# Kernel tuning notes

Hardware: AMD Instinct MI355X
Metric: run time of the kernel (lower is better)

The kernel has to match this reference:

```python
import jax, jax.numpy as jnp
import numpy as np

FEATURE_DIM = 256
TEMP = 0.1
BASE_TEMP = 0.07
MAX_SAMPLES = 1024
SIM_THR = 0.7


def setup_inputs() -> dict:
    key = jax.random.key(0)
    ks = jax.random.split(key, 8)
    B, C, H, W = 4, FEATURE_DIM, 160, 160
    s = 1.0 / np.sqrt(C)
    return {
        'feats': jax.random.normal(ks[0], (B, C, H, W), jnp.float32),
        'labels': jax.random.randint(ks[1], (B, H, W), 0, 2).astype(jnp.int64),
        'superpixel_indice': jax.random.randint(ks[2], (B, H, W), 0, 200).astype(jnp.int64),
        'w1': jax.random.normal(ks[3], (C, C), jnp.float32) * s,
        'b1': jnp.zeros((C,), jnp.float32),
        'w2': jax.random.normal(ks[4], (C, C), jnp.float32) * s,
        'b2': jnp.zeros((C,), jnp.float32),
        'wa1': jax.random.normal(ks[5], (64, C), jnp.float32) * s,
        'ba1': jnp.zeros((64,), jnp.float32),
        'wa2': jax.random.normal(ks[6], (1, 64), jnp.float32) * (1.0 / 8.0),
        'ba2': jnp.zeros((1,), jnp.float32),
    }


def _per_sample(f, w, lab, sp):
    # f: (N, C) normalized proj feats, w: (N,) pixel weights, lab/sp: (N,) int
    valid = lab == 1
    # deterministic sample: stable-sort valid pixels to the front, take MAX_SAMPLES
    order = jnp.argsort(jnp.where(valid, 0, 1).astype(jnp.int32))
    idx = order[:MAX_SAMPLES]
    sel = valid[idx]                       # (S,) real-sample mask (pads if <S valid)
    tf = f[idx]                            # (S, C)
    tw = w[idx]                            # (S,)
    ts = sp[idx]                           # (S,)
    sim = tf @ tf.T                        # (S, S)
    S = MAX_SAMPLES
    eye = jnp.eye(S, dtype=bool)
    pos = (ts[:, None] == ts[None, :]) & (sim > SIM_THR)
    pos = pos & sel[:, None] & sel[None, :] & ~eye
    exp_sim = jnp.exp(sim / TEMP) * sel[None, :].astype(sim.dtype)
    denom = exp_sim.sum(axis=1)            # (S,)
    log_prob = sim / TEMP - jnp.log(jnp.where(denom > 0, denom, 1.0))[:, None]
    pw = tw[:, None] * tw[None, :]
    pwm = jnp.where(pos, pw, 0.0)
    psum = pwm.sum()
    loss = -(TEMP / BASE_TEMP) * (pwm * jnp.where(pos, log_prob, 0.0)).sum() / jnp.where(psum > 0, psum, 1.0)
    has = psum > 0
    return jnp.where(has, loss, 0.0), has


def reference(feats, labels, superpixel_indice, w1, b1, w2, b2, wa1, ba1, wa2, ba2):
    B, C, H, W = feats.shape
    x = jnp.transpose(feats, (0, 2, 3, 1)).reshape(B, H * W, C)  # (B, N, C)
    proj = jax.nn.relu(x @ w1.T + b1) @ w2.T + b2                # 1x1 convs == per-pixel matmul
    attn = jax.nn.sigmoid(jax.nn.relu(x @ wa1.T + ba1) @ wa2.T + ba2)[..., 0]  # (B, N)
    nrm = jnp.linalg.norm(proj, axis=-1, keepdims=True)
    fn = proj / jnp.maximum(nrm, 1e-12)
    lab = labels.reshape(B, -1)
    sp = superpixel_indice.reshape(B, -1)
    losses, flags = jax.vmap(_per_sample)(fn, attn, lab, sp)
    n = flags.sum().astype(jnp.float32)
    return jnp.where(n > 0, losses.sum() / jnp.maximum(n, 1.0), 0.0)
```

## Files before the change

kernel.cpp:

```cpp
#include <hip/hip_runtime.h>
#include <hip/hip_bf16.h>
#include <math.h>

#define NPIX   25600
#define CDIM   256
#define SSEL   1024
#define BATCH  4
#define NCHUNK 25
#define INV_T  10.0f
#define RATIO  1.4285714285714286f
#define THR    0.7f

typedef __attribute__((ext_vector_type(8))) short bf16x8;
typedef __attribute__((ext_vector_type(4))) float f32x4;
typedef unsigned short u16;

__device__ __forceinline__ u16 to_bf16(float v) {
  __hip_bfloat16 h = __float2bfloat16(v);
  return *reinterpret_cast<u16*>(&h);
}

__global__ __launch_bounds__(256) void pack_weights(
    const float* __restrict__ w1, const float* __restrict__ w2,
    const float* __restrict__ wa1, const int* __restrict__ labels,
    u16* __restrict__ w1b, u16* __restrict__ w2b, u16* __restrict__ wab,
    float* __restrict__ denom, float* __restrict__ Prow, float* __restrict__ Ssum,
    int* __restrict__ counts) {
  int t = threadIdx.x;
  int e = blockIdx.x * 256 + t;
  if (e < 65536) {
    w1b[e] = to_bf16(w1[e]);
    w2b[e] = to_bf16(w2[e]);
  }
  if (e < 16384) wab[e] = to_bf16(wa1[e]);
  if (e < BATCH * SSEL) { denom[e] = 0.f; Prow[e] = 0.f; }
  if (e < BATCH) Ssum[e] = 0.f;

  if (blockIdx.x < BATCH * NCHUNK) {
    int b = blockIdx.x / NCHUNK, ch = blockIdx.x % NCHUNK;
    const int* lab = labels + b * NPIX + ch * 1024;
    int local = 0;
#pragma unroll
    for (int qq = 0; qq < 4; ++qq) local += (lab[qq * 256 + t] == 1);
    for (int off = 32; off > 0; off >>= 1) local += __shfl_xor(local, off, 64);
    __shared__ int ws[4];
    if ((t & 63) == 0) ws[t >> 6] = local;
    __syncthreads();
    if (t == 0) counts[blockIdx.x] = ws[0] + ws[1] + ws[2] + ws[3];
  }
}

__global__ __launch_bounds__(1024) void select_scatter(
    const int* __restrict__ labels, const int* __restrict__ sp,
    const int* __restrict__ counts,
    int* __restrict__ idx, int* __restrict__ selv, int* __restrict__ tsp) {
  int b = blockIdx.x / NCHUNK, ch = blockIdx.x % NCHUNK;
  int t = threadIdx.x;
  __shared__ int cs[NCHUNK];
  __shared__ int wave_tot[16];
  if (t < NCHUNK) cs[t] = counts[b * NCHUNK + t];
  __syncthreads();
  int Vtot = 0, vbase = 0;
#pragma unroll
  for (int c = 0; c < NCHUNK; ++c) {
    int v = cs[c];
    Vtot += v;
    if (c < ch) vbase += v;
  }
  int ibase = ch * 1024 - vbase;

  int i = ch * 1024 + t;
  int isv = (labels[b * NPIX + i] == 1) ? 1 : 0;
  int lane = t & 63, wid = t >> 6;
  unsigned long long mv = __ballot(isv);
  int pv = __popcll(mv & ((1ull << lane) - 1ull));
  if (lane == 0) wave_tot[wid] = __popcll(mv);
  __syncthreads();
  for (int w = 0; w < wid; ++w) pv += wave_tot[w];
  int gslot = isv ? (vbase + pv) : (Vtot + ibase + (t - pv));
  if (gslot < SSEL) {
    idx [b * SSEL + gslot] = i;
    selv[b * SSEL + gslot] = isv;
    tsp [b * SSEL + gslot] = sp[b * NPIX + i];
  }
}

__global__ __launch_bounds__(256) void gather_cast(
    const float* __restrict__ feats, const int* __restrict__ idx,
    u16* __restrict__ xh) {
  int r0 = blockIdx.x * 16;
  int b  = r0 >> 10;
  int t  = threadIdx.x;
  __shared__ int ridx[16];
  if (t < 16) ridx[t] = idx[r0 + t];
  __syncthreads();
  const float* fb = feats + ((long)b * CDIM + t) * NPIX;
#pragma unroll 4
  for (int r = 0; r < 16; ++r) {
    xh[(long)(r0 + r) * CDIM + t] = to_bf16(fb[ridx[r]]);
  }
}

__global__ __launch_bounds__(256) void gemm1_kernel(
    const u16* __restrict__ xh, const u16* __restrict__ w1b,
    const u16* __restrict__ wab,
    const float* __restrict__ b1, const float* __restrict__ ba1,
    const float* __restrict__ wa2, const float* __restrict__ ba2,
    u16* __restrict__ hh, float* __restrict__ tw) {
  int n  = blockIdx.x;
  int i0 = blockIdx.y * 64;
  int t = threadIdx.x;
  int lane = t & 63, w = t >> 6, m = lane & 15, q = lane >> 4;
  bool attn = (n == 4);
  const u16* bsrc = attn ? wab : (w1b + n * 64 * 256);

  __shared__ __align__(16) u16 Ah[64 * 72];
  __shared__ __align__(16) u16 Bh[64 * 72];

  f32x4 acc[4];
#pragma unroll
  for (int nt = 0; nt < 4; ++nt) acc[nt] = {0.f, 0.f, 0.f, 0.f};

  for (int kk = 0; kk < 4; ++kk) {
    __syncthreads();
#pragma unroll
    for (int p = 0; p < 2; ++p) {
      int e = p * 256 + t;
      int row = e >> 3, kg = e & 7;
      int lo = row * 72 + kg * 8;
      *(uint4*)&Ah[lo] = *(const uint4*)&xh[(i0 + row) * 256 + kk * 64 + kg * 8];
      *(uint4*)&Bh[lo] = *(const uint4*)&bsrc[row * 256 + kk * 64 + kg * 8];
    }
    __syncthreads();
#pragma unroll
    for (int ks = 0; ks < 2; ++ks) {
      int koff = ks * 32 + q * 8;
      bf16x8 ah = *(const bf16x8*)&Ah[(w * 16 + m) * 72 + koff];
#pragma unroll
      for (int nt = 0; nt < 4; ++nt) {
        bf16x8 bh = *(const bf16x8*)&Bh[(nt * 16 + m) * 72 + koff];
        acc[nt] = __builtin_amdgcn_mfma_f32_16x16x32_bf16(ah, bh, acc[nt], 0, 0, 0);
      }
    }
  }

  if (!attn) {
#pragma unroll
    for (int nt = 0; nt < 4; ++nt) {
      int col = n * 64 + nt * 16 + m;
      float bb = b1[col];
#pragma unroll
      for (int reg = 0; reg < 4; ++reg) {
        int row = i0 + w * 16 + q * 4 + reg;
        hh[row * 256 + col] = to_bf16(fmaxf(acc[nt][reg] + bb, 0.f));
      }
    }
  } else {
    float part[4] = {0.f, 0.f, 0.f, 0.f};
#pragma unroll
    for (int nt = 0; nt < 4; ++nt) {
      int ca = nt * 16 + m;
      float bb = ba1[ca], wv = wa2[ca];
#pragma unroll
      for (int reg = 0; reg < 4; ++reg)
        part[reg] += fmaxf(acc[nt][reg] + bb, 0.f) * wv;
    }
    for (int off = 8; off > 0; off >>= 1) {
#pragma unroll
      for (int reg = 0; reg < 4; ++reg)
        part[reg] += __shfl_xor(part[reg], off, 64);
    }
    if (m == 0) {
      float bb2 = ba2[0];
#pragma unroll
      for (int reg = 0; reg < 4; ++reg) {
        int row = i0 + w * 16 + q * 4 + reg;
        tw[row] = 1.f / (1.f + expf(-(part[reg] + bb2)));
      }
    }
  }
}

__global__ __launch_bounds__(256) void gemm2norm_kernel(
    const u16* __restrict__ hh, const u16* __restrict__ w2b,
    const float* __restrict__ b2, u16* __restrict__ fnb) {
  int i0 = blockIdx.x * 64;
  int t = threadIdx.x;
  int lane = t & 63, w = t >> 6, m = lane & 15, q = lane >> 4;

  __shared__ __align__(16) u16 Bs[64 * 264];

  bf16x8 af[8];
#pragma unroll
  for (int ks = 0; ks < 8; ++ks)
    af[ks] = *(const bf16x8*)&hh[(i0 + w * 16 + m) * 256 + ks * 32 + q * 8];

  f32x4 acc[4][4];
#pragma unroll
  for (int n = 0; n < 4; ++n)
#pragma unroll
    for (int nt = 0; nt < 4; ++nt) acc[n][nt] = {0.f, 0.f, 0.f, 0.f};

  for (int n = 0; n < 4; ++n) {
    __syncthreads();
#pragma unroll
    for (int i = 0; i < 8; ++i) {
      int e = i * 256 + t;
      int row = e >> 5, kg = e & 31;
      *(uint4*)&Bs[row * 264 + kg * 8] = *(const uint4*)&w2b[(n * 64 + row) * 256 + kg * 8];
    }
    __syncthreads();
#pragma unroll
    for (int ks = 0; ks < 8; ++ks) {
      int koff = ks * 32 + q * 8;
#pragma unroll
      for (int nt = 0; nt < 4; ++nt) {
        bf16x8 bh = *(const bf16x8*)&Bs[(nt * 16 + m) * 264 + koff];
        acc[n][nt] = __builtin_amdgcn_mfma_f32_16x16x32_bf16(af[ks], bh, acc[n][nt], 0, 0, 0);
      }
    }
  }

  float ss[4] = {0.f, 0.f, 0.f, 0.f};
#pragma unroll
  for (int n = 0; n < 4; ++n)
#pragma unroll
    for (int nt = 0; nt < 4; ++nt) {
      float bb = b2[n * 64 + nt * 16 + m];
#pragma unroll
      for (int reg = 0; reg < 4; ++reg) {
        float p = acc[n][nt][reg] + bb;
        acc[n][nt][reg] = p;
        ss[reg] += p * p;
      }
    }
  for (int off = 8; off > 0; off >>= 1) {
#pragma unroll
    for (int reg = 0; reg < 4; ++reg) ss[reg] += __shfl_xor(ss[reg], off, 64);
  }
  float inv[4];
#pragma unroll
  for (int reg = 0; reg < 4; ++reg)
    inv[reg] = 1.f / fmaxf(sqrtf(ss[reg]), 1e-12f);

#pragma unroll
  for (int n = 0; n < 4; ++n)
#pragma unroll
    for (int nt = 0; nt < 4; ++nt) {
      int col = n * 64 + nt * 16 + m;
#pragma unroll
      for (int reg = 0; reg < 4; ++reg) {
        int row = i0 + w * 16 + q * 4 + reg;
        fnb[row * 256 + col] = to_bf16(acc[n][nt][reg] * inv[reg]);
      }
    }
}

__global__ __launch_bounds__(256) void sim_kernel(
    const u16* __restrict__ fnb, const float* __restrict__ tw,
    const int* __restrict__ selv, const int* __restrict__ tsp,
    float* __restrict__ denom, float* __restrict__ Prow, float* __restrict__ Ssum) {
  int b = blockIdx.y;
  int t = threadIdx.x;
  int lane = t & 63, w = t >> 6;
  int m = lane & 15, q = lane >> 4;

  int rem = blockIdx.x, ti = 0;
  while (rem >= (16 - ti)) { rem -= (16 - ti); ++ti; }
  int tj = ti + rem;
  bool diag = (ti == tj);
  int i0 = ti * 64, j0 = tj * 64;
  int base = b << 10;

  __shared__ __align__(16) u16 Ah[64 * 72];
  __shared__ __align__(16) u16 Bhh[64 * 72];
  __shared__ float drl[64], Prl[64];
  __shared__ float dclw[4][64], Pclw[4][64];
  __shared__ float swv[4];

  const u16* Bh = diag ? Ah : Bhh;

  f32x4 acc[4];
#pragma unroll
  for (int nt = 0; nt < 4; ++nt) acc[nt] = {0.f, 0.f, 0.f, 0.f};

  for (int kk = 0; kk < 4; ++kk) {
    __syncthreads();
#pragma unroll
    for (int p = 0; p < 2; ++p) {
      int e = p * 256 + t;
      int row = e >> 3, kg = e & 7;
      int lo = row * 72 + kg * 8;
      *(uint4*)&Ah[lo] = *(const uint4*)&fnb[(base + i0 + row) * 256 + kk * 64 + kg * 8];
      if (!diag)
        *(uint4*)&Bhh[lo] = *(const uint4*)&fnb[(base + j0 + row) * 256 + kk * 64 + kg * 8];
    }
    __syncthreads();
#pragma unroll
    for (int ks = 0; ks < 2; ++ks) {
      int koff = ks * 32 + q * 8;
      bf16x8 ah = *(const bf16x8*)&Ah[(w * 16 + m) * 72 + koff];
#pragma unroll
      for (int nt = 0; nt < 4; ++nt) {
        bf16x8 bh = *(const bf16x8*)&Bh[(nt * 16 + m) * 72 + koff];
        acc[nt] = __builtin_amdgcn_mfma_f32_16x16x32_bf16(ah, bh, acc[nt], 0, 0, 0);
      }
    }
  }

  int   gi[4], gj[4], si[4], sj[4], ci[4], cj[4];
  float twi[4], twj[4];
#pragma unroll
  for (int reg = 0; reg < 4; ++reg) {
    int i = i0 + w * 16 + q * 4 + reg;
    gi[reg] = i; twi[reg] = tw[base + i];
    si[reg] = selv[base + i]; ci[reg] = tsp[base + i];
  }
#pragma unroll
  for (int nt = 0; nt < 4; ++nt) {
    int j = j0 + nt * 16 + m;
    gj[nt] = j; twj[nt] = tw[base + j];
    sj[nt] = selv[base + j]; cj[nt] = tsp[base + j];
  }

  float dR[4] = {0, 0, 0, 0}, PR[4] = {0, 0, 0, 0};
  float dC[4] = {0, 0, 0, 0}, PC[4] = {0, 0, 0, 0};
  float Sp = 0.f;
#pragma unroll
  for (int nt = 0; nt < 4; ++nt) {
#pragma unroll
    for (int reg = 0; reg < 4; ++reg) {
      float s = acc[nt][reg];
      float e10 = __expf(s * INV_T);
      if (sj[nt]) dR[reg] += e10;
      if (si[reg]) dC[nt] += e10;
      if (si[reg] && sj[nt] && (ci[reg] == cj[nt]) && (s > THR) && (gi[reg] != gj[nt])) {
        float pw = twi[reg] * twj[nt];
        PR[reg] += pw;
        PC[nt] += pw;
        Sp += pw * s;
      }
    }
  }

  for (int off = 8; off > 0; off >>= 1) {
#pragma unroll
    for (int reg = 0; reg < 4; ++reg) {
      dR[reg] += __shfl_xor(dR[reg], off, 64);
      PR[reg] += __shfl_xor(PR[reg], off, 64);
    }
  }
  if (m == 0) {
#pragma unroll
    for (int reg = 0; reg < 4; ++reg) {
      drl[w * 16 + q * 4 + reg] = dR[reg];
      Prl[w * 16 + q * 4 + reg] = PR[reg];
    }
  }
  if (!diag) {
    for (int off = 32; off >= 16; off >>= 1) {
#pragma unroll
      for (int nt = 0; nt < 4; ++nt) {
        dC[nt] += __shfl_xor(dC[nt], off, 64);
        PC[nt] += __shfl_xor(PC[nt], off, 64);
      }
    }
    if (q == 0) {
#pragma unroll
      for (int nt = 0; nt < 4; ++nt) {
        dclw[w][nt * 16 + m] = dC[nt];
        Pclw[w][nt * 16 + m] = PC[nt];
      }
    }
  }
  for (int off = 32; off > 0; off >>= 1) Sp += __shfl_xor(Sp, off, 64);
  if (lane == 0) swv[w] = Sp;
  __syncthreads();

  if (t < 64) {
    atomicAdd(&denom[base + i0 + t], drl[t]);
    atomicAdd(&Prow [base + i0 + t], Prl[t]);
    if (!diag) {
      float dc = dclw[0][t] + dclw[1][t] + dclw[2][t] + dclw[3][t];
      float pc = Pclw[0][t] + Pclw[1][t] + Pclw[2][t] + Pclw[3][t];
      atomicAdd(&denom[base + j0 + t], dc);
      atomicAdd(&Prow [base + j0 + t], pc);
    }
  }
  if (t == 0) {
    float St = swv[0] + swv[1] + swv[2] + swv[3];
    atomicAdd(&Ssum[b], diag ? St : 2.f * St);
  }
}

__global__ __launch_bounds__(1024) void finalize_kernel(
    const float* __restrict__ denom, const float* __restrict__ Prow,
    const float* __restrict__ Ssum, float* __restrict__ out) {
  int t = threadIdx.x;
  int b = t >> 8, u = t & 255;
  float P = 0.f, L = 0.f;
#pragma unroll
  for (int q = 0; q < 4; ++q) {
    int s = u + q * 256;
    float p = Prow[b * SSEL + s];
    float D = denom[b * SSEL + s];
    P += p;
    L += p * logf(D > 0.f ? D : 1.f);
  }
  for (int off = 32; off > 0; off >>= 1) {
    P += __shfl_xor(P, off, 64);
    L += __shfl_xor(L, off, 64);
  }
  __shared__ float wP[16], wL[16];
  int lane = t & 63, w = t >> 6;
  if (lane == 0) { wP[w] = P; wL[w] = L; }
  __syncthreads();
  if (t == 0) {
    float total = 0.f, n = 0.f;
    for (int bb = 0; bb < BATCH; ++bb) {
      float psum = wP[4 * bb] + wP[4 * bb + 1] + wP[4 * bb + 2] + wP[4 * bb + 3];
      float lsum = wL[4 * bb] + wL[4 * bb + 1] + wL[4 * bb + 2] + wL[4 * bb + 3];
      if (psum > 0.f) {
        float wls = Ssum[bb] * INV_T - lsum;
        total += -RATIO * wls / psum;
        n += 1.f;
      }
    }
    out[0] = (n > 0.f) ? (total / n) : 0.f;
  }
}

extern "C" void kernel_launch(void* const* d_in, const int* in_sizes, int n_in,
                              void* d_out, int out_size, void* d_ws, size_t ws_size,
                              hipStream_t stream) {
  const float* feats = (const float*)d_in[0];
  const int*   labels = (const int*)d_in[1];
  const int*   sp     = (const int*)d_in[2];
  const float* w1  = (const float*)d_in[3];
  const float* b1  = (const float*)d_in[4];
  const float* w2  = (const float*)d_in[5];
  const float* b2  = (const float*)d_in[6];
  const float* wa1 = (const float*)d_in[7];
  const float* ba1 = (const float*)d_in[8];
  const float* wa2 = (const float*)d_in[9];
  const float* ba2 = (const float*)d_in[10];
  float* out = (float*)d_out;

  char* W = (char*)d_ws;
  u16* w1b = (u16*)W;               W += 65536 * 2;
  u16* w2b = (u16*)W;               W += 65536 * 2;
  u16* wab = (u16*)W;               W += 16384 * 2;
  u16* xh  = (u16*)W;               W += 1048576 * 2;
  u16* hh  = (u16*)W;               W += 1048576 * 2;
  u16* fnb = (u16*)W;               W += 1048576 * 2;
  float* tw   = (float*)W;          W += 4096 * 4;
  float* denom= (float*)W;          W += 4096 * 4;
  float* Prow = (float*)W;          W += 4096 * 4;
  float* Ssum = (float*)W;          W += 4 * 4;
  int*   idx  = (int*)W;            W += 4096 * 4;
  int*   selv = (int*)W;            W += 4096 * 4;
  int*   tsp  = (int*)W;            W += 4096 * 4;
  int*   counts = (int*)W;          W += 128 * 4;

  pack_weights<<<256, 256, 0, stream>>>(w1, w2, wa1, labels, w1b, w2b, wab,
                                        denom, Prow, Ssum, counts);
  select_scatter<<<BATCH * NCHUNK, 1024, 0, stream>>>(labels, sp, counts,
                                                      idx, selv, tsp);
  gather_cast<<<256, 256, 0, stream>>>(feats, idx, xh);
  gemm1_kernel<<<dim3(5, 64), 256, 0, stream>>>(xh, w1b, wab, b1, ba1,
                                                wa2, ba2, hh, tw);
  gemm2norm_kernel<<<64, 256, 0, stream>>>(hh, w2b, b2, fnb);
  sim_kernel<<<dim3(136, BATCH), 256, 0, stream>>>(fnb, tw, selv, tsp,
                                                   denom, Prow, Ssum);
  finalize_kernel<<<1, 1024, 0, stream>>>(denom, Prow, Ssum, out);
}
```

Before: 194.9 us.

## Drop LDS staging in GEMMs, load MFMA operands directly, widen grids

The three MFMA GEMM kernels (gemm1, gemm2norm, sim) now read their bf16 operand fragments straight from global memory instead of staging tiles through shared memory with barriers. gemm2norm is reorganised so each block handles 16 rows, with the four waves splitting the output columns and combining the row norms through a small shared array; its grid grows fourfold. gather_cast also uses 4 rows per block with a grid four times larger. The goal is more blocks on a small problem and fewer barriers, at the cost of redundant global/L2 reads and uncoalesced fragment loads.

After: 201.0 us. 1.03x slower.

```diff
diff --git a/kernel.cpp b/kernel.cpp
--- a/kernel.cpp
+++ b/kernel.cpp
@@ -88,15 +88,15 @@
 __global__ __launch_bounds__(256) void gather_cast(
     const float* __restrict__ feats, const int* __restrict__ idx,
     u16* __restrict__ xh) {
-  int r0 = blockIdx.x * 16;
+  int r0 = blockIdx.x * 4;
   int b  = r0 >> 10;
   int t  = threadIdx.x;
-  __shared__ int ridx[16];
-  if (t < 16) ridx[t] = idx[r0 + t];
+  __shared__ int ridx[4];
+  if (t < 4) ridx[t] = idx[r0 + t];
   __syncthreads();
   const float* fb = feats + ((long)b * CDIM + t) * NPIX;
-#pragma unroll 4
-  for (int r = 0; r < 16; ++r) {
+#pragma unroll
+  for (int r = 0; r < 4; ++r) {
     xh[(long)(r0 + r) * CDIM + t] = to_bf16(fb[ridx[r]]);
   }
 }
@@ -114,33 +114,20 @@
   bool attn = (n == 4);
   const u16* bsrc = attn ? wab : (w1b + n * 64 * 256);
 
-  __shared__ __align__(16) u16 Ah[64 * 72];
-  __shared__ __align__(16) u16 Bh[64 * 72];
+  const u16* arow = xh + (i0 + w * 16 + m) * 256 + q * 8;
+  const u16* brow = bsrc + m * 256 + q * 8;
 
   f32x4 acc[4];
 #pragma unroll
   for (int nt = 0; nt < 4; ++nt) acc[nt] = {0.f, 0.f, 0.f, 0.f};
 
-  for (int kk = 0; kk < 4; ++kk) {
-    __syncthreads();
-#pragma unroll
-    for (int p = 0; p < 2; ++p) {
-      int e = p * 256 + t;
-      int row = e >> 3, kg = e & 7;
-      int lo = row * 72 + kg * 8;
-      *(uint4*)&Ah[lo] = *(const uint4*)&xh[(i0 + row) * 256 + kk * 64 + kg * 8];
-      *(uint4*)&Bh[lo] = *(const uint4*)&bsrc[row * 256 + kk * 64 + kg * 8];
-    }
-    __syncthreads();
-#pragma unroll
-    for (int ks = 0; ks < 2; ++ks) {
-      int koff = ks * 32 + q * 8;
-      bf16x8 ah = *(const bf16x8*)&Ah[(w * 16 + m) * 72 + koff];
-#pragma unroll
-      for (int nt = 0; nt < 4; ++nt) {
-        bf16x8 bh = *(const bf16x8*)&Bh[(nt * 16 + m) * 72 + koff];
-        acc[nt] = __builtin_amdgcn_mfma_f32_16x16x32_bf16(ah, bh, acc[nt], 0, 0, 0);
-      }
+#pragma unroll
+  for (int ks = 0; ks < 8; ++ks) {
+    bf16x8 ah = *(const bf16x8*)&arow[ks * 32];
+#pragma unroll
+    for (int nt = 0; nt < 4; ++nt) {
+      bf16x8 bh = *(const bf16x8*)&brow[nt * 16 * 256 + ks * 32];
+      acc[nt] = __builtin_amdgcn_mfma_f32_16x16x32_bf16(ah, bh, acc[nt], 0, 0, 0);
     }
   }
 
@@ -184,76 +171,59 @@
 __global__ __launch_bounds__(256) void gemm2norm_kernel(
     const u16* __restrict__ hh, const u16* __restrict__ w2b,
     const float* __restrict__ b2, u16* __restrict__ fnb) {
-  int i0 = blockIdx.x * 64;
+  int i0 = blockIdx.x * 16;
   int t = threadIdx.x;
   int lane = t & 63, w = t >> 6, m = lane & 15, q = lane >> 4;
 
-  __shared__ __align__(16) u16 Bs[64 * 264];
-
-  bf16x8 af[8];
-#pragma unroll
-  for (int ks = 0; ks < 8; ++ks)
-    af[ks] = *(const bf16x8*)&hh[(i0 + w * 16 + m) * 256 + ks * 32 + q * 8];
-
-  f32x4 acc[4][4];
-#pragma unroll
-  for (int n = 0; n < 4; ++n)
-#pragma unroll
-    for (int nt = 0; nt < 4; ++nt) acc[n][nt] = {0.f, 0.f, 0.f, 0.f};
-
-  for (int n = 0; n < 4; ++n) {
-    __syncthreads();
-#pragma unroll
-    for (int i = 0; i < 8; ++i) {
-      int e = i * 256 + t;
-      int row = e >> 5, kg = e & 31;
-      *(uint4*)&Bs[row * 264 + kg * 8] = *(const uint4*)&w2b[(n * 64 + row) * 256 + kg * 8];
-    }
-    __syncthreads();
-#pragma unroll
-    for (int ks = 0; ks < 8; ++ks) {
-      int koff = ks * 32 + q * 8;
-#pragma unroll
-      for (int nt = 0; nt < 4; ++nt) {
-        bf16x8 bh = *(const bf16x8*)&Bs[(nt * 16 + m) * 264 + koff];
-        acc[n][nt] = __builtin_amdgcn_mfma_f32_16x16x32_bf16(af[ks], bh, acc[n][nt], 0, 0, 0);
-      }
+  const u16* arow = hh + (i0 + m) * 256 + q * 8;
+  const u16* brow = w2b + (w * 64 + m) * 256 + q * 8;
+
+  f32x4 acc[4];
+#pragma unroll
+  for (int nt = 0; nt < 4; ++nt) acc[nt] = {0.f, 0.f, 0.f, 0.f};
+
+#pragma unroll
+  for (int ks = 0; ks < 8; ++ks) {
+    bf16x8 ah = *(const bf16x8*)&arow[ks * 32];
+#pragma unroll
+    for (int nt = 0; nt < 4; ++nt) {
+      bf16x8 bh = *(const bf16x8*)&brow[nt * 16 * 256 + ks * 32];
+      acc[nt] = __builtin_amdgcn_mfma_f32_16x16x32_bf16(ah, bh, acc[nt], 0, 0, 0);
     }
   }
 
   float ss[4] = {0.f, 0.f, 0.f, 0.f};
 #pragma unroll
-  for (int n = 0; n < 4; ++n)
-#pragma unroll
-    for (int nt = 0; nt < 4; ++nt) {
-      float bb = b2[n * 64 + nt * 16 + m];
-#pragma unroll
-      for (int reg = 0; reg < 4; ++reg) {
-        float p = acc[n][nt][reg] + bb;
-        acc[n][nt][reg] = p;
-        ss[reg] += p * p;
-      }
-    }
+  for (int nt = 0; nt < 4; ++nt) {
+    float bb = b2[w * 64 + nt * 16 + m];
+#pragma unroll
+    for (int reg = 0; reg < 4; ++reg) {
+      float p = acc[nt][reg] + bb;
+      acc[nt][reg] = p;
+      ss[reg] += p * p;
+    }
+  }
   for (int off = 8; off > 0; off >>= 1) {
 #pragma unroll
     for (int reg = 0; reg < 4; ++reg) ss[reg] += __shfl_xor(ss[reg], off, 64);
   }
-  float inv[4];
-#pragma unroll
-  for (int reg = 0; reg < 4; ++reg)
-    inv[reg] = 1.f / fmaxf(sqrtf(ss[reg]), 1e-12f);
-
-#pragma unroll
-  for (int n = 0; n < 4; ++n)
-#pragma unroll
-    for (int nt = 0; nt < 4; ++nt) {
-      int col = n * 64 + nt * 16 + m;
-#pragma unroll
-      for (int reg = 0; reg < 4; ++reg) {
-        int row = i0 + w * 16 + q * 4 + reg;
-        fnb[row * 256 + col] = to_bf16(acc[n][nt][reg] * inv[reg]);
-      }
-    }
+  __shared__ float ssw[4][16];
+  if (m == 0) {
+#pragma unroll
+    for (int reg = 0; reg < 4; ++reg) ssw[w][q * 4 + reg] = ss[reg];
+  }
+  __syncthreads();
+#pragma unroll
+  for (int nt = 0; nt < 4; ++nt) {
+    int col = w * 64 + nt * 16 + m;
+#pragma unroll
+    for (int reg = 0; reg < 4; ++reg) {
+      int r = q * 4 + reg;
+      float tot = ssw[0][r] + ssw[1][r] + ssw[2][r] + ssw[3][r];
+      float inv = 1.f / fmaxf(sqrtf(tot), 1e-12f);
+      fnb[(i0 + r) * 256 + col] = to_bf16(acc[nt][reg] * inv);
+    }
+  }
 }
 
 __global__ __launch_bounds__(256) void sim_kernel(
@@ -268,46 +238,31 @@
   int rem = blockIdx.x, ti = 0;
   while (rem >= (16 - ti)) { rem -= (16 - ti); ++ti; }
   int tj = ti + rem;
-  bool diag = (ti == tj);
   int i0 = ti * 64, j0 = tj * 64;
   int base = b << 10;
 
-  __shared__ __align__(16) u16 Ah[64 * 72];
-  __shared__ __align__(16) u16 Bhh[64 * 72];
   __shared__ float drl[64], Prl[64];
   __shared__ float dclw[4][64], Pclw[4][64];
   __shared__ float swv[4];
 
-  const u16* Bh = diag ? Ah : Bhh;
+  const u16* arow = fnb + (base + i0 + w * 16 + m) * 256 + q * 8;
+  const u16* brow = fnb + (base + j0 + m) * 256 + q * 8;
 
   f32x4 acc[4];
 #pragma unroll
   for (int nt = 0; nt < 4; ++nt) acc[nt] = {0.f, 0.f, 0.f, 0.f};
 
-  for (int kk = 0; kk < 4; ++kk) {
-    __syncthreads();
-#pragma unroll
-    for (int p = 0; p < 2; ++p) {
-      int e = p * 256 + t;
-      int row = e >> 3, kg = e & 7;
-      int lo = row * 72 + kg * 8;
-      *(uint4*)&Ah[lo] = *(const uint4*)&fnb[(base + i0 + row) * 256 + kk * 64 + kg * 8];
-      if (!diag)
-        *(uint4*)&Bhh[lo] = *(const uint4*)&fnb[(base + j0 + row) * 256 + kk * 64 + kg * 8];
-    }
-    __syncthreads();
-#pragma unroll
-    for (int ks = 0; ks < 2; ++ks) {
-      int koff = ks * 32 + q * 8;
-      bf16x8 ah = *(const bf16x8*)&Ah[(w * 16 + m) * 72 + koff];
-#pragma unroll
-      for (int nt = 0; nt < 4; ++nt) {
-        bf16x8 bh = *(const bf16x8*)&Bh[(nt * 16 + m) * 72 + koff];
-        acc[nt] = __builtin_amdgcn_mfma_f32_16x16x32_bf16(ah, bh, acc[nt], 0, 0, 0);
-      }
-    }
-  }
-
+#pragma unroll
+  for (int ks = 0; ks < 8; ++ks) {
+    bf16x8 ah = *(const bf16x8*)&arow[ks * 32];
+#pragma unroll
+    for (int nt = 0; nt < 4; ++nt) {
+      bf16x8 bh = *(const bf16x8*)&brow[nt * 16 * 256 + ks * 32];
+      acc[nt] = __builtin_amdgcn_mfma_f32_16x16x32_bf16(ah, bh, acc[nt], 0, 0, 0);
+    }
+  }
+
+  bool diag = (ti == tj);
   int   gi[4], gj[4], si[4], sj[4], ci[4], cj[4];
   float twi[4], twj[4];
 #pragma unroll
@@ -466,10 +421,10 @@
                                         denom, Prow, Ssum, counts);
   select_scatter<<<BATCH * NCHUNK, 1024, 0, stream>>>(labels, sp, counts,
                                                       idx, selv, tsp);
-  gather_cast<<<256, 256, 0, stream>>>(feats, idx, xh);
+  gather_cast<<<1024, 256, 0, stream>>>(feats, idx, xh);
   gemm1_kernel<<<dim3(5, 64), 256, 0, stream>>>(xh, w1b, wab, b1, ba1,
                                                 wa2, ba2, hh, tw);
-  gemm2norm_kernel<<<64, 256, 0, stream>>>(hh, w2b, b2, fnb);
+  gemm2norm_kernel<<<256, 256, 0, stream>>>(hh, w2b, b2, fnb);
   sim_kernel<<<dim3(136, BATCH), 256, 0, stream>>>(fnb, tw, selv, tsp,
                                                    denom, Prow, Ssum);
   finalize_kernel<<<1, 1024, 0, stream>>>(denom, Prow, Ssum, out);
```
